# Kernel optimization log

Hardware: AMD Instinct MI355X
Metric: run time of the kernel (lower is better)

Reference implementation:

```python
import jax, jax.numpy as jnp
import numpy as np

NUM_EXPERTS = 8
NUM_LANGS = 4
TOP_K = 2
D_MODEL = 1024
EXPERT_SIZE = 4096
B, S = 2, 2048


def setup_inputs() -> dict:
    key = jax.random.key(0)
    ks = jax.random.split(key, 6)
    def xavier(k, shape, fan_in, fan_out):
        a = float(np.sqrt(6.0 / (fan_in + fan_out)))
        return jax.random.uniform(k, shape, jnp.float32, -a, a)
    return {
        "x": jax.random.normal(ks[0], (B, S, D_MODEL), jnp.float32),
        "router_w": xavier(ks[1], (NUM_EXPERTS, D_MODEL), D_MODEL, NUM_EXPERTS),
        "router_b": jnp.zeros((NUM_EXPERTS,), jnp.float32),
        "lang_w": xavier(ks[2], (NUM_LANGS, D_MODEL), D_MODEL, NUM_LANGS),
        "lang_b": jnp.zeros((NUM_LANGS,), jnp.float32),
        "w1": xavier(ks[3], (NUM_EXPERTS, D_MODEL, EXPERT_SIZE), D_MODEL, EXPERT_SIZE),
        "b1": jnp.zeros((NUM_EXPERTS, EXPERT_SIZE), jnp.float32),
        "w2": xavier(ks[4], (NUM_EXPERTS, EXPERT_SIZE, D_MODEL), EXPERT_SIZE, D_MODEL),
        "b2": jnp.zeros((NUM_EXPERTS, D_MODEL), jnp.float32),
    }


def reference(x, router_w, router_b, lang_w, lang_b, w1, b1, w2, b2):
    # Language-aware routing bias
    lang_logits = x @ lang_w.T + lang_b                      # [B,S,L]
    lang_probs = jax.nn.softmax(lang_logits, axis=-1)
    # lang_probs[..., idx:idx+2].sum(-1): slice may be width 1 at the edge,
    # emulate with a zero pad column.
    lp_pad = jnp.pad(lang_probs, ((0, 0), (0, 0), (0, 1)))
    idx = jnp.arange(NUM_EXPERTS) % NUM_LANGS                # [E]
    expert_weights = lp_pad[..., idx] + lp_pad[..., idx + 1] # [B,S,E]

    router_logits = x @ router_w.T + router_b + 0.1 * expert_weights
    router_probs = jax.nn.softmax(router_logits, axis=-1)   # [B,S,E]
    top_p, top_i = jax.lax.top_k(router_probs, TOP_K)        # [B,S,K]
    top_p = top_p / top_p.sum(axis=-1, keepdims=True)

    # Dense per-expert MLP (dropout=0 / eval). torch GELU default = exact erf.
    h = jax.nn.gelu(jnp.einsum('bsd,edh->bseh', x, w1) + b1, approximate=False)
    expert_out = jnp.einsum('bseh,ehd->bsed', h, w2) + b2    # [B,S,E,D]

    sel = jnp.take_along_axis(expert_out, top_i[..., None], axis=2)  # [B,S,K,D]
    return (top_p[..., None] * sel).sum(axis=2)              # [B,S,D]
```

## Files before the change

kernel.cpp:

```cpp
#include <hip/hip_runtime.h>
#include <cstdint>
#include <cstddef>

#define T_TOK 4096
#define DM 1024
#define HS 4096
#define NE 8
#define MAXROWS 9216
#define MAXTILES 72

typedef __attribute__((ext_vector_type(8))) short short8;
typedef __attribute__((ext_vector_type(4))) float floatx4;

__device__ __forceinline__ unsigned short f2bf(float f) {
  union { float f; unsigned u; } v; v.f = f;
  unsigned r = (v.u + 0x7fffu + ((v.u >> 16) & 1u)) >> 16;
  return (unsigned short)r;
}

__device__ __forceinline__ void gload_lds16(const void* g, void* l) {
  __builtin_amdgcn_global_load_lds((const __attribute__((address_space(1))) void*)g,
                                   (__attribute__((address_space(3))) void*)l, 16, 0, 0);
}


__global__ void k_init(int* counts, int* cursor, unsigned* list) {
  int i = blockIdx.x * 256 + threadIdx.x;
  if (i < NE) { counts[i] = 0; cursor[i] = 0; }
  if (i < MAXROWS) list[i] = 0xFFFFFFFFu;
}

__global__ void k_route(const float* __restrict__ x, const float* __restrict__ rw,
                        const float* __restrict__ rb, const float* __restrict__ lw,
                        const float* __restrict__ lb, int* __restrict__ top_i,
                        float* __restrict__ top_p, int* __restrict__ counts) {
  int t = blockIdx.x * 4 + (threadIdx.x >> 6);
  int lane = threadIdx.x & 63;
  const float4* xt = (const float4*)(x + (size_t)t * DM);
  float4 xv[4];
#pragma unroll
  for (int j = 0; j < 4; j++) xv[j] = xt[lane * 4 + j];
  float dots[12];
#pragma unroll
  for (int r = 0; r < 12; r++) {
    const float4* wr = (const float4*)(r < 4 ? lw + r * DM : rw + (r - 4) * DM);
    float s = 0.f;
#pragma unroll
    for (int j = 0; j < 4; j++) {
      float4 w = wr[lane * 4 + j];
      s += xv[j].x * w.x + xv[j].y * w.y + xv[j].z * w.z + xv[j].w * w.w;
    }
#pragma unroll
    for (int o = 32; o > 0; o >>= 1) s += __shfl_xor(s, o, 64);
    dots[r] = s;
  }
  if (lane == 0) {
    float lp[4]; float m = -1e30f;
#pragma unroll
    for (int i = 0; i < 4; i++) { lp[i] = dots[i] + lb[i]; m = fmaxf(m, lp[i]); }
    float sum = 0.f;
#pragma unroll
    for (int i = 0; i < 4; i++) { lp[i] = expf(lp[i] - m); sum += lp[i]; }
#pragma unroll
    for (int i = 0; i < 4; i++) lp[i] /= sum;
    float ew[4];
    ew[0] = lp[0] + lp[1]; ew[1] = lp[1] + lp[2]; ew[2] = lp[2] + lp[3]; ew[3] = lp[3];
    float r8[8];
#pragma unroll
    for (int e = 0; e < 8; e++) r8[e] = dots[4 + e] + rb[e] + 0.1f * ew[e & 3];
    int e0 = 0;
#pragma unroll
    for (int e = 1; e < 8; e++) if (r8[e] > r8[e0]) e0 = e;
    int e1 = (e0 == 0) ? 1 : 0;
#pragma unroll
    for (int e = 0; e < 8; e++) if (e != e0 && r8[e] > r8[e1]) e1 = e;
    float tt = expf(r8[e1] - r8[e0]);
    float w0 = 1.f / (1.f + tt);
    float w1 = tt / (1.f + tt);
    top_i[t * 2] = e0; top_i[t * 2 + 1] = e1;
    top_p[t * 2] = w0; top_p[t * 2 + 1] = w1;
    atomicAdd(&counts[e0], 1); atomicAdd(&counts[e1], 1);
  }
}

__global__ void k_offsets(const int* counts, int* off) {
  if (threadIdx.x == 0) {
    int acc = 0;
    for (int e = 0; e < NE; e++) {
      off[e] = acc;
      int p = ((counts[e] + 127) >> 7) << 7;
      acc += p;
    }
    off[NE] = acc;
  }
}

__global__ void k_scatter(const int* __restrict__ top_i, const int* __restrict__ off,
                          int* cursor, unsigned* __restrict__ list) {
  int t = blockIdx.x * 256 + threadIdx.x;
  if (t >= T_TOK) return;
#pragma unroll
  for (int k = 0; k < 2; k++) {
    int e = top_i[t * 2 + k];
    int pos = atomicAdd(&cursor[e], 1);
    list[off[e] + pos] = (unsigned)(t * 2 + k);
  }
}

__global__ void k_cvt_x(const float* __restrict__ x, unsigned short* __restrict__ xb) {
  int i = blockIdx.x * 256 + threadIdx.x;
  float4 v = ((const float4*)x)[i];
  union { unsigned short us[4]; uint2 u2; } o;
  o.us[0] = f2bf(v.x); o.us[1] = f2bf(v.y); o.us[2] = f2bf(v.z); o.us[3] = f2bf(v.w);
  ((uint2*)xb)[i] = o.u2;
}

__global__ void k_transpose_bf16(const float* __restrict__ src, unsigned short* __restrict__ dst,
                                 int K, int N) {
  __shared__ float tile[64][65];
  const float* s = src + (size_t)blockIdx.z * K * N;
  unsigned short* d = dst + (size_t)blockIdx.z * K * N;
  int n0 = blockIdx.x * 64, k0 = blockIdx.y * 64;
  int tr = threadIdx.x >> 4;
  int tc = (threadIdx.x & 15) * 4;
#pragma unroll
  for (int j = 0; j < 4; j++) {
    int row = tr + j * 16;
    float4 v = *(const float4*)&s[(size_t)(k0 + row) * N + n0 + tc];
    tile[row][tc + 0] = v.x; tile[row][tc + 1] = v.y;
    tile[row][tc + 2] = v.z; tile[row][tc + 3] = v.w;
  }
  __syncthreads();
#pragma unroll
  for (int j = 0; j < 4; j++) {
    int n = tr + j * 16;
    union { unsigned short us[4]; uint2 u2; } o;
#pragma unroll
    for (int i = 0; i < 4; i++) o.us[i] = f2bf(tile[tc + i][n]);
    *(uint2*)&d[(size_t)(n0 + n) * K + k0 + tc] = o.u2;
  }
}

__global__ void k_init_out(const int* __restrict__ top_i, const float* __restrict__ top_p,
                           const float* __restrict__ b2, float* __restrict__ out) {
  int i = blockIdx.x * 256 + threadIdx.x;
  int t = i >> 10, d = i & 1023;
  int e0 = top_i[t * 2], e1 = top_i[t * 2 + 1];
  out[i] = top_p[t * 2] * b2[e0 * DM + d] + top_p[t * 2 + 1] * b2[e1 * DM + d];
}

template <int MODE>
__global__ __launch_bounds__(256, 4) void k_gemm(
    const unsigned short* __restrict__ Abase,
    const unsigned short* __restrict__ Wt,
    const int* __restrict__ off, const unsigned* __restrict__ list,
    const float* __restrict__ b1, const float* __restrict__ top_p,
    unsigned short* __restrict__ Hout, float* __restrict__ out,
    int K, int N) {
  int nx = gridDim.x;
  int flat = blockIdx.y * nx + blockIdx.x;
  int cpx = (nx * gridDim.y) >> 3;
  int swz = (flat & 7) * cpx + (flat >> 3);
  int n0 = (swz % nx) * 128;
  int r0 = (swz / nx) * 128;

  int total = off[NE];
  if (r0 >= total) return;
  int e = 0;
  while (r0 >= off[e + 1]) ++e;

  __shared__ __align__(16) unsigned short lA[2][128 * 32];
  __shared__ __align__(16) unsigned short lB[2][128 * 32];
  __shared__ float sP[128];
  __shared__ int sTok[128];

  int tid = threadIdx.x;
  int srow = tid >> 2;
  int key_s = (srow >> 1) & 3;
  int koff_src = (((tid & 3) ^ key_s) * 8);
  int kdst = (tid & 3) * 8;

  const unsigned short* srcA[2];
#pragma unroll
  for (int c = 0; c < 2; c++) {
    int row = c * 64 + srow;
    size_t arow;
    if (MODE == 0) {
      unsigned pair = list[r0 + row];
      arow = (pair == 0xFFFFFFFFu) ? 0 : (size_t)(pair >> 1);
    } else {
      arow = (size_t)(r0 + row);
    }
    srcA[c] = Abase + arow * K + koff_src;
  }
  const unsigned short* srcB[2];
#pragma unroll
  for (int c = 0; c < 2; c++)
    srcB[c] = Wt + ((size_t)e * N + n0 + c * 64 + srow) * K + koff_src;

  if (MODE == 1 && tid < 128) {
    unsigned pair = list[r0 + tid];
    if (pair == 0xFFFFFFFFu) { sTok[tid] = -1; sP[tid] = 0.f; }
    else { sTok[tid] = (int)(pair >> 1); sP[tid] = top_p[pair]; }
  }

  floatx4 acc[4][4] = {};
  int lane = tid & 63;
  int w = tid >> 6;
  int wm = w >> 1, wn = w & 1;
  int lr = lane & 15, kq = lane >> 4;
  int kx = kq ^ ((lr >> 1) & 3);

#define STAGE(BUF, KK)                                                        \
  do {                                                                        \
    _Pragma("unroll")                                                         \
    for (int c = 0; c < 2; c++) {                                             \
      gload_lds16(srcA[c] + (KK), &lA[BUF][(c * 64 + srow) * 32 + kdst]);     \
      gload_lds16(srcB[c] + (KK), &lB[BUF][(c * 64 + srow) * 32 + kdst]);     \
    }                                                                         \
  } while (0)

  STAGE(0, 0);
  __syncthreads();

  int cur = 0;
  for (int k0 = 0; k0 < K; k0 += 32) {
    if (k0 + 32 < K) STAGE(cur ^ 1, k0 + 32);
    const short8* pA = (const short8*)lA[cur];
    const short8* pB = (const short8*)lB[cur];
    short8 a[4], b[4];
#pragma unroll
    for (int i = 0; i < 4; i++) a[i] = pA[(wm * 64 + i * 16 + lr) * 4 + kx];
#pragma unroll
    for (int j = 0; j < 4; j++) b[j] = pB[(wn * 64 + j * 16 + lr) * 4 + kx];
#pragma unroll
    for (int i = 0; i < 4; i++)
#pragma unroll
      for (int j = 0; j < 4; j++)
        acc[i][j] = __builtin_amdgcn_mfma_f32_16x16x32_bf16(a[i], b[j], acc[i][j], 0, 0, 0);
    __syncthreads();
    cur ^= 1;
  }
#undef STAGE

  int rbase = wm * 64 + kq * 4;
  int cbase = wn * 64 + lr;
  if (MODE == 0) {
#pragma unroll
    for (int i = 0; i < 4; i++)
#pragma unroll
      for (int j = 0; j < 4; j++)
#pragma unroll
        for (int g = 0; g < 4; g++) {
          int row = rbase + i * 16 + g;
          int col = cbase + j * 16;
          float v = acc[i][j][g] + b1[e * HS + n0 + col];
          v = 0.5f * v * (1.f + erff(v * 0.70710678118f));
          Hout[(size_t)(r0 + row) * (size_t)N + n0 + col] = f2bf(v);
        }
  } else {
#pragma unroll
    for (int i = 0; i < 4; i++)
#pragma unroll
      for (int j = 0; j < 4; j++)
#pragma unroll
        for (int g = 0; g < 4; g++) {
          int row = rbase + i * 16 + g;
          int col = cbase + j * 16;
          int tok = sTok[row];
          if (tok >= 0)
            atomicAdd(&out[(size_t)tok * DM + n0 + col], sP[row] * acc[i][j][g]);
        }
  }
}


extern "C" void kernel_launch(void* const* d_in, const int* in_sizes, int n_in,
                              void* d_out, int out_size, void* d_ws, size_t ws_size,
                              hipStream_t stream) {
  const float* x  = (const float*)d_in[0];
  const float* rw = (const float*)d_in[1];
  const float* rb = (const float*)d_in[2];
  const float* lw = (const float*)d_in[3];
  const float* lb = (const float*)d_in[4];
  const float* w1 = (const float*)d_in[5];
  const float* b1 = (const float*)d_in[6];
  const float* w2 = (const float*)d_in[7];
  const float* b2 = (const float*)d_in[8];
  float* out = (float*)d_out;
  char* ws = (char*)d_ws;

  int* counts = (int*)ws;
  int* cursor = (int*)(ws + 32);
  int* off    = (int*)(ws + 64);
  int* top_i  = (int*)(ws + 128);
  float* top_p = (float*)(ws + 128 + 32768);
  unsigned* list = (unsigned*)(ws + 65792);
  unsigned short* xb = (unsigned short*)(ws + 102912);
  unsigned short* wt = (unsigned short*)(ws + 102912 + 8388608);
  unsigned short* h  = (unsigned short*)(ws + 102912 + 8388608 + 67108864);

  k_init<<<dim3((MAXROWS + 255) / 256), dim3(256), 0, stream>>>(counts, cursor, list);
  k_route<<<dim3(T_TOK / 4), dim3(256), 0, stream>>>(x, rw, rb, lw, lb, top_i, top_p, counts);
  k_offsets<<<dim3(1), dim3(64), 0, stream>>>(counts, off);
  k_scatter<<<dim3(T_TOK / 256), dim3(256), 0, stream>>>(top_i, off, cursor, list);
  k_cvt_x<<<dim3(T_TOK * DM / 4 / 256), dim3(256), 0, stream>>>(x, xb);
  k_transpose_bf16<<<dim3(HS / 64, DM / 64, NE), dim3(256), 0, stream>>>(w1, wt, DM, HS);
  k_gemm<0><<<dim3(HS / 128, MAXTILES), dim3(256), 0, stream>>>(
      xb, wt, off, list, b1, top_p, h, nullptr, DM, HS);
  k_transpose_bf16<<<dim3(DM / 64, HS / 64, NE), dim3(256), 0, stream>>>(w2, wt, HS, DM);
  k_init_out<<<dim3(T_TOK * DM / 256), dim3(256), 0, stream>>>(top_i, top_p, b2, out);
  k_gemm<1><<<dim3(DM / 128, MAXTILES), dim3(256), 0, stream>>>(
      h, wt, off, list, nullptr, top_p, nullptr, out, HS, DM);
}
```

Before: 515.4 us.

## Triple-buffer GEMM pipeline, split-K the second GEMM, fuse x conversion, tanh GELU

The GEMM now uses three LDS stages with explicit vmcnt waits and split A/B staging interleaved with MFMA groups under s_setprio. K and N become template constants. The second GEMM is split four ways along K across gridDim.z to add parallelism, and its results are still combined through atomics. The x-to-bf16 conversion is fused into the init kernel, and the exact erf GELU is replaced with a tanh approximation, which changes numerics and may not match the reference.

Measured after the change: 541.5 us. 1.05x slower.

```diff
diff --git a/kernel.cpp b/kernel.cpp
--- a/kernel.cpp
+++ b/kernel.cpp
@@ -24,10 +24,15 @@
 }
 
 
-__global__ void k_init(int* counts, int* cursor, unsigned* list) {
+__global__ void k_cvt_init(const float* __restrict__ x, unsigned short* __restrict__ xb,
+                           int* counts, int* cursor, unsigned* list) {
   int i = blockIdx.x * 256 + threadIdx.x;
   if (i < NE) { counts[i] = 0; cursor[i] = 0; }
   if (i < MAXROWS) list[i] = 0xFFFFFFFFu;
+  float4 v = ((const float4*)x)[i];
+  union { unsigned short us[4]; uint2 u2; } o;
+  o.us[0] = f2bf(v.x); o.us[1] = f2bf(v.y); o.us[2] = f2bf(v.z); o.us[3] = f2bf(v.w);
+  ((uint2*)xb)[i] = o.u2;
 }
 
 __global__ void k_route(const float* __restrict__ x, const float* __restrict__ rw,
@@ -107,14 +112,6 @@
   }
 }
 
-__global__ void k_cvt_x(const float* __restrict__ x, unsigned short* __restrict__ xb) {
-  int i = blockIdx.x * 256 + threadIdx.x;
-  float4 v = ((const float4*)x)[i];
-  union { unsigned short us[4]; uint2 u2; } o;
-  o.us[0] = f2bf(v.x); o.us[1] = f2bf(v.y); o.us[2] = f2bf(v.z); o.us[3] = f2bf(v.w);
-  ((uint2*)xb)[i] = o.u2;
-}
-
 __global__ void k_transpose_bf16(const float* __restrict__ src, unsigned short* __restrict__ dst,
                                  int K, int N) {
   __shared__ float tile[64][65];
@@ -149,36 +146,39 @@
   out[i] = top_p[t * 2] * b2[e0 * DM + d] + top_p[t * 2 + 1] * b2[e1 * DM + d];
 }
 
-template <int MODE>
-__global__ __launch_bounds__(256, 4) void k_gemm(
+template <int MODE, int K, int N, int KT>
+__global__ __launch_bounds__(256, 3) void k_gemm(
     const unsigned short* __restrict__ Abase,
     const unsigned short* __restrict__ Wt,
     const int* __restrict__ off, const unsigned* __restrict__ list,
-    const float* __restrict__ b1, const float* __restrict__ top_p,
-    unsigned short* __restrict__ Hout, float* __restrict__ out,
-    int K, int N) {
-  int nx = gridDim.x;
-  int flat = blockIdx.y * nx + blockIdx.x;
-  int cpx = (nx * gridDim.y) >> 3;
+    const float* __restrict__ bias, const float* __restrict__ top_p,
+    unsigned short* __restrict__ Hout, float* __restrict__ out) {
+  int gx = gridDim.x, gy = gridDim.y;
+  int flat = (blockIdx.z * gy + blockIdx.y) * gx + blockIdx.x;
+  int nwg = gx * gy * gridDim.z;
+  int cpx = nwg >> 3;
   int swz = (flat & 7) * cpx + (flat >> 3);
-  int n0 = (swz % nx) * 128;
-  int r0 = (swz / nx) * 128;
+  int bn = swz % gx; int rest = swz / gx;
+  int bm = rest % gy; int zz = rest / gy;
+  int n0 = bn * 128;
+  int r0 = bm * 128;
+  int kb = zz * (KT * 32);
 
   int total = off[NE];
   if (r0 >= total) return;
   int e = 0;
   while (r0 >= off[e + 1]) ++e;
 
-  __shared__ __align__(16) unsigned short lA[2][128 * 32];
-  __shared__ __align__(16) unsigned short lB[2][128 * 32];
+  __shared__ __align__(16) unsigned short lA[3][128 * 32];
+  __shared__ __align__(16) unsigned short lB[3][128 * 32];
   __shared__ float sP[128];
   __shared__ int sTok[128];
 
   int tid = threadIdx.x;
   int srow = tid >> 2;
-  int key_s = (srow >> 1) & 3;
-  int koff_src = (((tid & 3) ^ key_s) * 8);
-  int kdst = (tid & 3) * 8;
+  int skey = (srow >> 1) & 3;
+  int koff_src = ((tid & 3) ^ skey) * 8;
+  int ldst = srow * 32 + (tid & 3) * 8;
 
   const unsigned short* srcA[2];
 #pragma unroll
@@ -191,12 +191,12 @@
     } else {
       arow = (size_t)(r0 + row);
     }
-    srcA[c] = Abase + arow * K + koff_src;
+    srcA[c] = Abase + arow * K + kb + koff_src;
   }
   const unsigned short* srcB[2];
 #pragma unroll
   for (int c = 0; c < 2; c++)
-    srcB[c] = Wt + ((size_t)e * N + n0 + c * 64 + srow) * K + koff_src;
+    srcB[c] = Wt + ((size_t)e * N + n0 + c * 64 + srow) * K + kb + koff_src;
 
   if (MODE == 1 && tid < 128) {
     unsigned pair = list[r0 + tid];
@@ -210,38 +210,66 @@
   int wm = w >> 1, wn = w & 1;
   int lr = lane & 15, kq = lane >> 4;
   int kx = kq ^ ((lr >> 1) & 3);
-
-#define STAGE(BUF, KK)                                                        \
+  int aBase = (wm * 64 + lr) * 4 + kx;
+  int bBase = (wn * 64 + lr) * 4 + kx;
+
+#define STAGE_A(BUF, TT)                                                      \
   do {                                                                        \
     _Pragma("unroll")                                                         \
-    for (int c = 0; c < 2; c++) {                                             \
-      gload_lds16(srcA[c] + (KK), &lA[BUF][(c * 64 + srow) * 32 + kdst]);     \
-      gload_lds16(srcB[c] + (KK), &lB[BUF][(c * 64 + srow) * 32 + kdst]);     \
-    }                                                                         \
+    for (int c = 0; c < 2; c++)                                               \
+      gload_lds16(srcA[c] + (size_t)(TT) * 32, &lA[BUF][c * 2048 + ldst]);    \
   } while (0)
-
-  STAGE(0, 0);
+#define STAGE_B(BUF, TT)                                                      \
+  do {                                                                        \
+    _Pragma("unroll")                                                         \
+    for (int c = 0; c < 2; c++)                                               \
+      gload_lds16(srcB[c] + (size_t)(TT) * 32, &lB[BUF][c * 2048 + ldst]);    \
+  } while (0)
+
   __syncthreads();
 
-  int cur = 0;
-  for (int k0 = 0; k0 < K; k0 += 32) {
-    if (k0 + 32 < K) STAGE(cur ^ 1, k0 + 32);
+  STAGE_A(0, 0); STAGE_B(0, 0);
+  STAGE_A(1, 1); STAGE_B(1, 1);
+  asm volatile("s_waitcnt vmcnt(4)\ns_barrier" ::: "memory");
+
+  int cur = 0, nxt = 2;
+  for (int t = 0; t < KT; ++t) {
     const short8* pA = (const short8*)lA[cur];
     const short8* pB = (const short8*)lB[cur];
-    short8 a[4], b[4];
-#pragma unroll
-    for (int i = 0; i < 4; i++) a[i] = pA[(wm * 64 + i * 16 + lr) * 4 + kx];
-#pragma unroll
-    for (int j = 0; j < 4; j++) b[j] = pB[(wn * 64 + j * 16 + lr) * 4 + kx];
-#pragma unroll
-    for (int i = 0; i < 4; i++)
-#pragma unroll
-      for (int j = 0; j < 4; j++)
-        acc[i][j] = __builtin_amdgcn_mfma_f32_16x16x32_bf16(a[i], b[j], acc[i][j], 0, 0, 0);
-    __syncthreads();
-    cur ^= 1;
-  }
-#undef STAGE
+    bool pf = (t + 2 < KT);
+    if (pf) STAGE_A(nxt, t + 2);
+    short8 a0[4], b0[2];
+#pragma unroll
+    for (int m = 0; m < 4; m++) a0[m] = pA[aBase + m * 64];
+#pragma unroll
+    for (int n = 0; n < 2; n++) b0[n] = pB[bBase + n * 64];
+    __builtin_amdgcn_s_setprio(1);
+#pragma unroll
+    for (int m = 0; m < 4; m++)
+#pragma unroll
+      for (int n = 0; n < 2; n++)
+        acc[m][n] = __builtin_amdgcn_mfma_f32_16x16x32_bf16(a0[m], b0[n], acc[m][n], 0, 0, 0);
+    __builtin_amdgcn_s_setprio(0);
+    if (pf) STAGE_B(nxt, t + 2);
+    short8 b1v[2];
+#pragma unroll
+    for (int n = 0; n < 2; n++) b1v[n] = pB[bBase + (n + 2) * 64];
+    __builtin_amdgcn_s_setprio(1);
+#pragma unroll
+    for (int m = 0; m < 4; m++)
+#pragma unroll
+      for (int n = 0; n < 2; n++)
+        acc[m][n + 2] = __builtin_amdgcn_mfma_f32_16x16x32_bf16(a0[m], b1v[n], acc[m][n + 2], 0, 0, 0);
+    __builtin_amdgcn_s_setprio(0);
+    if (t + 1 < KT) {
+      if (pf) asm volatile("s_waitcnt vmcnt(4)\ns_barrier" ::: "memory");
+      else    asm volatile("s_waitcnt vmcnt(0)\ns_barrier" ::: "memory");
+    }
+    cur = (cur == 2) ? 0 : cur + 1;
+    nxt = (nxt == 2) ? 0 : nxt + 1;
+  }
+#undef STAGE_A
+#undef STAGE_B
 
   int rbase = wm * 64 + kq * 4;
   int cbase = wn * 64 + lr;
@@ -254,9 +282,10 @@
         for (int g = 0; g < 4; g++) {
           int row = rbase + i * 16 + g;
           int col = cbase + j * 16;
-          float v = acc[i][j][g] + b1[e * HS + n0 + col];
-          v = 0.5f * v * (1.f + erff(v * 0.70710678118f));
-          Hout[(size_t)(r0 + row) * (size_t)N + n0 + col] = f2bf(v);
+          float v = acc[i][j][g] + bias[e * N + n0 + col];
+          float u = v * (0.7978845608f + 0.0356774081f * v * v);
+          float gl = v / (1.f + __expf(-2.f * u));
+          Hout[(size_t)(r0 + row) * (size_t)N + n0 + col] = f2bf(gl);
         }
   } else {
 #pragma unroll
@@ -300,16 +329,15 @@
   unsigned short* wt = (unsigned short*)(ws + 102912 + 8388608);
   unsigned short* h  = (unsigned short*)(ws + 102912 + 8388608 + 67108864);
 
-  k_init<<<dim3((MAXROWS + 255) / 256), dim3(256), 0, stream>>>(counts, cursor, list);
+  k_cvt_init<<<dim3(T_TOK * DM / 4 / 256), dim3(256), 0, stream>>>(x, xb, counts, cursor, list);
   k_route<<<dim3(T_TOK / 4), dim3(256), 0, stream>>>(x, rw, rb, lw, lb, top_i, top_p, counts);
   k_offsets<<<dim3(1), dim3(64), 0, stream>>>(counts, off);
   k_scatter<<<dim3(T_TOK / 256), dim3(256), 0, stream>>>(top_i, off, cursor, list);
-  k_cvt_x<<<dim3(T_TOK * DM / 4 / 256), dim3(256), 0, stream>>>(x, xb);
   k_transpose_bf16<<<dim3(HS / 64, DM / 64, NE), dim3(256), 0, stream>>>(w1, wt, DM, HS);
-  k_gemm<0><<<dim3(HS / 128, MAXTILES), dim3(256), 0, stream>>>(
-      xb, wt, off, list, b1, top_p, h, nullptr, DM, HS);
+  k_init_out<<<dim3(T_TOK * DM / 256), dim3(256), 0, stream>>>(top_i, top_p, b2, out);
+  k_gemm<0, DM, HS, DM / 32><<<dim3(HS / 128, MAXTILES, 1), dim3(256), 0, stream>>>(
+      xb, wt, off, list, b1, top_p, h, nullptr);
   k_transpose_bf16<<<dim3(DM / 64, HS / 64, NE), dim3(256), 0, stream>>>(w2, wt, HS, DM);
-  k_init_out<<<dim3(T_TOK * DM / 256), dim3(256), 0, stream>>>(top_i, top_p, b2, out);
-  k_gemm<1><<<dim3(DM / 128, MAXTILES), dim3(256), 0, stream>>>(
-      h, wt, off, list, nullptr, top_p, nullptr, out, HS, DM);
-}
+  k_gemm<1, HS, DM, HS / 4 / 32><<<dim3(DM / 128, MAXTILES, 4), dim3(256), 0, stream>>>(
+      h, wt, off, list, nullptr, top_p, nullptr, out);
+}
```

## Fuse routing kernels, load gathered A from global, use tanh GELU

Applied to the files above, without the earlier changes.

Merges x bf16 conversion into the routing kernel, and merges offset computation and scatter into one single-block kernel. Replaces the init kernel with memsets. Splits the templated GEMM into two kernels. The first GEMM now reads gathered A rows directly from global memory into registers instead of staging them through LDS. It also replaces the exact erf GELU with a tanh/sigmoid approximation, which changes numerics relative to the reference's exact GELU. Together these aim to cut launch overhead, LDS traffic and epilogue cost.

New measurement: 583.9 us. 13.3% more time.

```diff
diff --git a/kernel.cpp b/kernel.cpp
--- a/kernel.cpp
+++ b/kernel.cpp
@@ -23,17 +23,19 @@
                                    (__attribute__((address_space(3))) void*)l, 16, 0, 0);
 }
 
-
-__global__ void k_init(int* counts, int* cursor, unsigned* list) {
-  int i = blockIdx.x * 256 + threadIdx.x;
-  if (i < NE) { counts[i] = 0; cursor[i] = 0; }
-  if (i < MAXROWS) list[i] = 0xFFFFFFFFu;
-}
-
-__global__ void k_route(const float* __restrict__ x, const float* __restrict__ rw,
-                        const float* __restrict__ rb, const float* __restrict__ lw,
-                        const float* __restrict__ lb, int* __restrict__ top_i,
-                        float* __restrict__ top_p, int* __restrict__ counts) {
+__global__ void k_cvt_route(const float* __restrict__ x, unsigned short* __restrict__ xb,
+                            const float* __restrict__ rw, const float* __restrict__ rb,
+                            const float* __restrict__ lw, const float* __restrict__ lb,
+                            int* __restrict__ top_i, float* __restrict__ top_p,
+                            int* __restrict__ counts) {
+#pragma unroll
+  for (int j = 0; j < 4; j++) {
+    int i = blockIdx.x * 1024 + j * 256 + threadIdx.x;
+    float4 v = ((const float4*)x)[i];
+    union { unsigned short us[4]; uint2 u2; } o;
+    o.us[0] = f2bf(v.x); o.us[1] = f2bf(v.y); o.us[2] = f2bf(v.z); o.us[3] = f2bf(v.w);
+    ((uint2*)xb)[i] = o.u2;
+  }
   int t = blockIdx.x * 4 + (threadIdx.x >> 6);
   int lane = threadIdx.x & 63;
   const float4* xt = (const float4*)(x + (size_t)t * DM);
@@ -83,36 +85,26 @@
   }
 }
 
-__global__ void k_offsets(const int* counts, int* off) {
+__global__ void k_offscatter(const int* __restrict__ counts, int* __restrict__ off,
+                             const int* __restrict__ top_i, int* cursor,
+                             unsigned* __restrict__ list) {
   if (threadIdx.x == 0) {
     int acc = 0;
     for (int e = 0; e < NE; e++) {
       off[e] = acc;
-      int p = ((counts[e] + 127) >> 7) << 7;
-      acc += p;
+      acc += ((counts[e] + 127) >> 7) << 7;
     }
     off[NE] = acc;
   }
-}
-
-__global__ void k_scatter(const int* __restrict__ top_i, const int* __restrict__ off,
-                          int* cursor, unsigned* __restrict__ list) {
-  int t = blockIdx.x * 256 + threadIdx.x;
-  if (t >= T_TOK) return;
-#pragma unroll
-  for (int k = 0; k < 2; k++) {
-    int e = top_i[t * 2 + k];
-    int pos = atomicAdd(&cursor[e], 1);
-    list[off[e] + pos] = (unsigned)(t * 2 + k);
-  }
-}
-
-__global__ void k_cvt_x(const float* __restrict__ x, unsigned short* __restrict__ xb) {
-  int i = blockIdx.x * 256 + threadIdx.x;
-  float4 v = ((const float4*)x)[i];
-  union { unsigned short us[4]; uint2 u2; } o;
-  o.us[0] = f2bf(v.x); o.us[1] = f2bf(v.y); o.us[2] = f2bf(v.z); o.us[3] = f2bf(v.w);
-  ((uint2*)xb)[i] = o.u2;
+  __syncthreads();
+  for (int t = threadIdx.x; t < T_TOK; t += 1024) {
+#pragma unroll
+    for (int k = 0; k < 2; k++) {
+      int e = top_i[t * 2 + k];
+      int pos = atomicAdd(&cursor[e], 1);
+      list[off[e] + pos] = (unsigned)(t * 2 + k);
+    }
+  }
 }
 
 __global__ void k_transpose_bf16(const float* __restrict__ src, unsigned short* __restrict__ dst,
@@ -149,14 +141,12 @@
   out[i] = top_p[t * 2] * b2[e0 * DM + d] + top_p[t * 2 + 1] * b2[e1 * DM + d];
 }
 
-template <int MODE>
-__global__ __launch_bounds__(256, 4) void k_gemm(
+__global__ __launch_bounds__(256, 4) void k_gemm1(
     const unsigned short* __restrict__ Abase,
     const unsigned short* __restrict__ Wt,
     const int* __restrict__ off, const unsigned* __restrict__ list,
-    const float* __restrict__ b1, const float* __restrict__ top_p,
-    unsigned short* __restrict__ Hout, float* __restrict__ out,
-    int K, int N) {
+    const float* __restrict__ bias, unsigned short* __restrict__ Hout) {
+  const int K = DM, N = HS;
   int nx = gridDim.x;
   int flat = blockIdx.y * nx + blockIdx.x;
   int cpx = (nx * gridDim.y) >> 3;
@@ -169,6 +159,101 @@
   int e = 0;
   while (r0 >= off[e + 1]) ++e;
 
+  __shared__ __align__(16) unsigned short lB[2][128 * 32];
+
+  int tid = threadIdx.x;
+  int srow = tid >> 2;
+  int key_s = (srow >> 1) & 3;
+  int koff_src = ((tid & 3) ^ key_s) * 8;
+  int kdst = (tid & 3) * 8;
+
+  const unsigned short* srcB[2];
+#pragma unroll
+  for (int c = 0; c < 2; c++)
+    srcB[c] = Wt + ((size_t)e * N + n0 + c * 64 + srow) * K + koff_src;
+
+  int lane = tid & 63;
+  int w = tid >> 6;
+  int wm = w >> 1, wn = w & 1;
+  int lr = lane & 15, kq = lane >> 4;
+  int kx = kq ^ ((lr >> 1) & 3);
+
+  unsigned aoff[4];
+#pragma unroll
+  for (int i = 0; i < 4; i++) {
+    int row = r0 + wm * 64 + i * 16 + lr;
+    unsigned pair = list[row];
+    unsigned arow = (pair == 0xFFFFFFFFu) ? 0u : (pair >> 1);
+    aoff[i] = arow * (unsigned)K + (unsigned)(kq * 8);
+  }
+
+  floatx4 acc[4][4] = {};
+
+#define STAGEB(BUF, KK)                                                       \
+  do {                                                                        \
+    _Pragma("unroll")                                                         \
+    for (int c = 0; c < 2; c++)                                               \
+      gload_lds16(srcB[c] + (KK), &lB[BUF][(c * 64 + srow) * 32 + kdst]);     \
+  } while (0)
+
+  STAGEB(0, 0);
+  __syncthreads();
+
+  int cur = 0;
+  for (int k0 = 0; k0 < K; k0 += 32) {
+    if (k0 + 32 < K) STAGEB(cur ^ 1, k0 + 32);
+    const short8* pB = (const short8*)lB[cur];
+    short8 a[4], b[4];
+#pragma unroll
+    for (int i = 0; i < 4; i++)
+      a[i] = *(const short8*)(Abase + aoff[i] + k0);
+#pragma unroll
+    for (int j = 0; j < 4; j++) b[j] = pB[(wn * 64 + j * 16 + lr) * 4 + kx];
+#pragma unroll
+    for (int i = 0; i < 4; i++)
+#pragma unroll
+      for (int j = 0; j < 4; j++)
+        acc[i][j] = __builtin_amdgcn_mfma_f32_16x16x32_bf16(a[i], b[j], acc[i][j], 0, 0, 0);
+    __syncthreads();
+    cur ^= 1;
+  }
+#undef STAGEB
+
+  int rbase = wm * 64 + kq * 4;
+  int cbase = wn * 64 + lr;
+#pragma unroll
+  for (int i = 0; i < 4; i++)
+#pragma unroll
+    for (int j = 0; j < 4; j++)
+#pragma unroll
+      for (int g = 0; g < 4; g++) {
+        int row = rbase + i * 16 + g;
+        int col = cbase + j * 16;
+        float v = acc[i][j][g] + bias[e * N + n0 + col];
+        float u = v * (0.7978845608f + 0.0356774081f * v * v);
+        float gl = v / (1.f + __expf(-2.f * u));
+        Hout[(size_t)(r0 + row) * (size_t)N + n0 + col] = f2bf(gl);
+      }
+}
+
+__global__ __launch_bounds__(256, 4) void k_gemm2(
+    const unsigned short* __restrict__ Abase,
+    const unsigned short* __restrict__ Wt,
+    const int* __restrict__ off, const unsigned* __restrict__ list,
+    const float* __restrict__ top_p, float* __restrict__ out) {
+  const int K = HS, N = DM;
+  int nx = gridDim.x;
+  int flat = blockIdx.y * nx + blockIdx.x;
+  int cpx = (nx * gridDim.y) >> 3;
+  int swz = (flat & 7) * cpx + (flat >> 3);
+  int n0 = (swz % nx) * 128;
+  int r0 = (swz / nx) * 128;
+
+  int total = off[NE];
+  if (r0 >= total) return;
+  int e = 0;
+  while (r0 >= off[e + 1]) ++e;
+
   __shared__ __align__(16) unsigned short lA[2][128 * 32];
   __shared__ __align__(16) unsigned short lB[2][128 * 32];
   __shared__ float sP[128];
@@ -177,28 +262,19 @@
   int tid = threadIdx.x;
   int srow = tid >> 2;
   int key_s = (srow >> 1) & 3;
-  int koff_src = (((tid & 3) ^ key_s) * 8);
+  int koff_src = ((tid & 3) ^ key_s) * 8;
   int kdst = (tid & 3) * 8;
 
   const unsigned short* srcA[2];
 #pragma unroll
-  for (int c = 0; c < 2; c++) {
-    int row = c * 64 + srow;
-    size_t arow;
-    if (MODE == 0) {
-      unsigned pair = list[r0 + row];
-      arow = (pair == 0xFFFFFFFFu) ? 0 : (size_t)(pair >> 1);
-    } else {
-      arow = (size_t)(r0 + row);
-    }
-    srcA[c] = Abase + arow * K + koff_src;
-  }
+  for (int c = 0; c < 2; c++)
+    srcA[c] = Abase + (size_t)(r0 + c * 64 + srow) * K + koff_src;
   const unsigned short* srcB[2];
 #pragma unroll
   for (int c = 0; c < 2; c++)
     srcB[c] = Wt + ((size_t)e * N + n0 + c * 64 + srow) * K + koff_src;
 
-  if (MODE == 1 && tid < 128) {
+  if (tid < 128) {
     unsigned pair = list[r0 + tid];
     if (pair == 0xFFFFFFFFu) { sTok[tid] = -1; sP[tid] = 0.f; }
     else { sTok[tid] = (int)(pair >> 1); sP[tid] = top_p[pair]; }
@@ -245,33 +321,18 @@
 
   int rbase = wm * 64 + kq * 4;
   int cbase = wn * 64 + lr;
-  if (MODE == 0) {
-#pragma unroll
-    for (int i = 0; i < 4; i++)
-#pragma unroll
-      for (int j = 0; j < 4; j++)
-#pragma unroll
-        for (int g = 0; g < 4; g++) {
-          int row = rbase + i * 16 + g;
-          int col = cbase + j * 16;
-          float v = acc[i][j][g] + b1[e * HS + n0 + col];
-          v = 0.5f * v * (1.f + erff(v * 0.70710678118f));
-          Hout[(size_t)(r0 + row) * (size_t)N + n0 + col] = f2bf(v);
-        }
-  } else {
-#pragma unroll
-    for (int i = 0; i < 4; i++)
-#pragma unroll
-      for (int j = 0; j < 4; j++)
-#pragma unroll
-        for (int g = 0; g < 4; g++) {
-          int row = rbase + i * 16 + g;
-          int col = cbase + j * 16;
-          int tok = sTok[row];
-          if (tok >= 0)
-            atomicAdd(&out[(size_t)tok * DM + n0 + col], sP[row] * acc[i][j][g]);
-        }
-  }
+#pragma unroll
+  for (int i = 0; i < 4; i++)
+#pragma unroll
+    for (int j = 0; j < 4; j++)
+#pragma unroll
+      for (int g = 0; g < 4; g++) {
+        int row = rbase + i * 16 + g;
+        int col = cbase + j * 16;
+        int tok = sTok[row];
+        if (tok >= 0)
+          atomicAdd(&out[(size_t)tok * DM + n0 + col], sP[row] * acc[i][j][g]);
+      }
 }
 
 
@@ -300,16 +361,16 @@
   unsigned short* wt = (unsigned short*)(ws + 102912 + 8388608);
   unsigned short* h  = (unsigned short*)(ws + 102912 + 8388608 + 67108864);
 
-  k_init<<<dim3((MAXROWS + 255) / 256), dim3(256), 0, stream>>>(counts, cursor, list);
-  k_route<<<dim3(T_TOK / 4), dim3(256), 0, stream>>>(x, rw, rb, lw, lb, top_i, top_p, counts);
-  k_offsets<<<dim3(1), dim3(64), 0, stream>>>(counts, off);
-  k_scatter<<<dim3(T_TOK / 256), dim3(256), 0, stream>>>(top_i, off, cursor, list);
-  k_cvt_x<<<dim3(T_TOK * DM / 4 / 256), dim3(256), 0, stream>>>(x, xb);
+  hipMemsetAsync(ws, 0, 128, stream);
+  hipMemsetAsync(list, 0xFF, MAXROWS * 4, stream);
+  k_cvt_route<<<dim3(T_TOK / 4), dim3(256), 0, stream>>>(
+      x, xb, rw, rb, lw, lb, top_i, top_p, counts);
+  k_offscatter<<<dim3(1), dim3(1024), 0, stream>>>(counts, off, top_i, cursor, list);
   k_transpose_bf16<<<dim3(HS / 64, DM / 64, NE), dim3(256), 0, stream>>>(w1, wt, DM, HS);
-  k_gemm<0><<<dim3(HS / 128, MAXTILES), dim3(256), 0, stream>>>(
-      xb, wt, off, list, b1, top_p, h, nullptr, DM, HS);
+  k_init_out<<<dim3(T_TOK * DM / 256), dim3(256), 0, stream>>>(top_i, top_p, b2, out);
+  k_gemm1<<<dim3(HS / 128, MAXTILES), dim3(256), 0, stream>>>(
+      xb, wt, off, list, b1, h);
   k_transpose_bf16<<<dim3(DM / 64, HS / 64, NE), dim3(256), 0, stream>>>(w2, wt, HS, DM);
-  k_init_out<<<dim3(T_TOK * DM / 256), dim3(256), 0, stream>>>(top_i, top_p, b2, out);
-  k_gemm<1><<<dim3(DM / 128, MAXTILES), dim3(256), 0, stream>>>(
-      h, wt, off, list, nullptr, top_p, nullptr, out, HS, DM);
-}
+  k_gemm2<<<dim3(DM / 128, MAXTILES), dim3(256), 0, stream>>>(
+      h, wt, off, list, top_p, out);
+}
```

## Fuse small setup kernels, widen weight transpose, vectorize init, use tanh GELU

Applied to the files above, without the earlier changes.

Merges the bf16 conversion of x into the routing kernel and folds the offset and scatter steps into one 1024-thread kernel. The init kernel is replaced with memsets. The fp32-to-bf16 weight transpose now works on 128x128 tiles, packs bf16 pairs with an XOR-swizzled LDS layout and writes 16-byte stores. The output-init kernel is vectorized to float4. The exact erf GELU in the first GEMM epilogue is replaced by a tanh-style approximation through __expf, which trades accuracy for fewer instructions.

New measurement: 523.8 us. No clear change (+1.6%).

```diff
diff --git a/kernel.cpp b/kernel.cpp
--- a/kernel.cpp
+++ b/kernel.cpp
@@ -23,17 +23,19 @@
                                    (__attribute__((address_space(3))) void*)l, 16, 0, 0);
 }
 
-
-__global__ void k_init(int* counts, int* cursor, unsigned* list) {
-  int i = blockIdx.x * 256 + threadIdx.x;
-  if (i < NE) { counts[i] = 0; cursor[i] = 0; }
-  if (i < MAXROWS) list[i] = 0xFFFFFFFFu;
-}
-
-__global__ void k_route(const float* __restrict__ x, const float* __restrict__ rw,
-                        const float* __restrict__ rb, const float* __restrict__ lw,
-                        const float* __restrict__ lb, int* __restrict__ top_i,
-                        float* __restrict__ top_p, int* __restrict__ counts) {
+__global__ void k_cvt_route(const float* __restrict__ x, unsigned short* __restrict__ xb,
+                            const float* __restrict__ rw, const float* __restrict__ rb,
+                            const float* __restrict__ lw, const float* __restrict__ lb,
+                            int* __restrict__ top_i, float* __restrict__ top_p,
+                            int* __restrict__ counts) {
+#pragma unroll
+  for (int j = 0; j < 4; j++) {
+    int i = blockIdx.x * 1024 + j * 256 + threadIdx.x;
+    float4 v = ((const float4*)x)[i];
+    union { unsigned short us[4]; uint2 u2; } o;
+    o.us[0] = f2bf(v.x); o.us[1] = f2bf(v.y); o.us[2] = f2bf(v.z); o.us[3] = f2bf(v.w);
+    ((uint2*)xb)[i] = o.u2;
+  }
   int t = blockIdx.x * 4 + (threadIdx.x >> 6);
   int lane = threadIdx.x & 63;
   const float4* xt = (const float4*)(x + (size_t)t * DM);
@@ -83,70 +85,74 @@
   }
 }
 
-__global__ void k_offsets(const int* counts, int* off) {
+__global__ void k_offscatter(const int* __restrict__ counts, int* __restrict__ off,
+                             const int* __restrict__ top_i, int* cursor,
+                             unsigned* __restrict__ list) {
   if (threadIdx.x == 0) {
     int acc = 0;
     for (int e = 0; e < NE; e++) {
       off[e] = acc;
-      int p = ((counts[e] + 127) >> 7) << 7;
-      acc += p;
+      acc += ((counts[e] + 127) >> 7) << 7;
     }
     off[NE] = acc;
   }
-}
-
-__global__ void k_scatter(const int* __restrict__ top_i, const int* __restrict__ off,
-                          int* cursor, unsigned* __restrict__ list) {
-  int t = blockIdx.x * 256 + threadIdx.x;
-  if (t >= T_TOK) return;
-#pragma unroll
-  for (int k = 0; k < 2; k++) {
-    int e = top_i[t * 2 + k];
-    int pos = atomicAdd(&cursor[e], 1);
-    list[off[e] + pos] = (unsigned)(t * 2 + k);
-  }
-}
-
-__global__ void k_cvt_x(const float* __restrict__ x, unsigned short* __restrict__ xb) {
-  int i = blockIdx.x * 256 + threadIdx.x;
-  float4 v = ((const float4*)x)[i];
-  union { unsigned short us[4]; uint2 u2; } o;
-  o.us[0] = f2bf(v.x); o.us[1] = f2bf(v.y); o.us[2] = f2bf(v.z); o.us[3] = f2bf(v.w);
-  ((uint2*)xb)[i] = o.u2;
-}
-
-__global__ void k_transpose_bf16(const float* __restrict__ src, unsigned short* __restrict__ dst,
-                                 int K, int N) {
-  __shared__ float tile[64][65];
+  __syncthreads();
+  for (int t = threadIdx.x; t < T_TOK; t += 1024) {
+#pragma unroll
+    for (int k = 0; k < 2; k++) {
+      int e = top_i[t * 2 + k];
+      int pos = atomicAdd(&cursor[e], 1);
+      list[off[e] + pos] = (unsigned)(t * 2 + k);
+    }
+  }
+}
+
+template <int K, int N>
+__global__ __launch_bounds__(256) void k_transpose2(const float* __restrict__ src,
+                                                    unsigned short* __restrict__ dst) {
+  __shared__ unsigned tile[128][68];
   const float* s = src + (size_t)blockIdx.z * K * N;
   unsigned short* d = dst + (size_t)blockIdx.z * K * N;
-  int n0 = blockIdx.x * 64, k0 = blockIdx.y * 64;
-  int tr = threadIdx.x >> 4;
-  int tc = (threadIdx.x & 15) * 4;
-#pragma unroll
-  for (int j = 0; j < 4; j++) {
-    int row = tr + j * 16;
-    float4 v = *(const float4*)&s[(size_t)(k0 + row) * N + n0 + tc];
-    tile[row][tc + 0] = v.x; tile[row][tc + 1] = v.y;
-    tile[row][tc + 2] = v.z; tile[row][tc + 3] = v.w;
+  int n0 = blockIdx.x * 128, k0 = blockIdx.y * 128;
+  int tid = threadIdx.x;
+  int nc4 = (tid & 31) * 4;
+  int kg = tid >> 5;
+#pragma unroll
+  for (int j = 0; j < 8; j++) {
+    int kp = kg + 8 * j;
+    int k = 2 * kp;
+    float4 a = *(const float4*)&s[(size_t)(k0 + k) * N + n0 + nc4];
+    float4 b = *(const float4*)&s[(size_t)(k0 + k + 1) * N + n0 + nc4];
+    const float* fa = (const float*)&a;
+    const float* fb = (const float*)&b;
+#pragma unroll
+    for (int i = 0; i < 4; i++) {
+      int n = nc4 + i;
+      int v = ((n >> 3) & 15) << 2;
+      tile[n][kp ^ v] = (unsigned)f2bf(fa[i]) | ((unsigned)f2bf(fb[i]) << 16);
+    }
   }
   __syncthreads();
-#pragma unroll
-  for (int j = 0; j < 4; j++) {
-    int n = tr + j * 16;
-    union { unsigned short us[4]; uint2 u2; } o;
-#pragma unroll
-    for (int i = 0; i < 4; i++) o.us[i] = f2bf(tile[tc + i][n]);
-    *(uint2*)&d[(size_t)(n0 + n) * K + k0 + tc] = o.u2;
+  int h = tid & 15;
+#pragma unroll
+  for (int j = 0; j < 8; j++) {
+    int n = (tid >> 4) + 16 * j;
+    int v = ((n >> 3) & 15) << 2;
+    uint4 q = *(const uint4*)&tile[n][(4 * h) ^ v];
+    *(uint4*)&d[(size_t)(n0 + n) * K + k0 + 8 * h] = q;
   }
 }
 
 __global__ void k_init_out(const int* __restrict__ top_i, const float* __restrict__ top_p,
-                           const float* __restrict__ b2, float* __restrict__ out) {
+                           const float* __restrict__ b2, float4* __restrict__ out) {
   int i = blockIdx.x * 256 + threadIdx.x;
-  int t = i >> 10, d = i & 1023;
+  int t = i >> 8, d4 = i & 255;
   int e0 = top_i[t * 2], e1 = top_i[t * 2 + 1];
-  out[i] = top_p[t * 2] * b2[e0 * DM + d] + top_p[t * 2 + 1] * b2[e1 * DM + d];
+  float p0 = top_p[t * 2], p1 = top_p[t * 2 + 1];
+  float4 b0 = ((const float4*)(b2 + e0 * DM))[d4];
+  float4 b1 = ((const float4*)(b2 + e1 * DM))[d4];
+  out[i] = make_float4(p0 * b0.x + p1 * b1.x, p0 * b0.y + p1 * b1.y,
+                       p0 * b0.z + p1 * b1.z, p0 * b0.w + p1 * b1.w);
 }
 
 template <int MODE>
@@ -154,7 +160,7 @@
     const unsigned short* __restrict__ Abase,
     const unsigned short* __restrict__ Wt,
     const int* __restrict__ off, const unsigned* __restrict__ list,
-    const float* __restrict__ b1, const float* __restrict__ top_p,
+    const float* __restrict__ bias, const float* __restrict__ top_p,
     unsigned short* __restrict__ Hout, float* __restrict__ out,
     int K, int N) {
   int nx = gridDim.x;
@@ -177,7 +183,7 @@
   int tid = threadIdx.x;
   int srow = tid >> 2;
   int key_s = (srow >> 1) & 3;
-  int koff_src = (((tid & 3) ^ key_s) * 8);
+  int koff_src = ((tid & 3) ^ key_s) * 8;
   int kdst = (tid & 3) * 8;
 
   const unsigned short* srcA[2];
@@ -254,9 +260,10 @@
         for (int g = 0; g < 4; g++) {
           int row = rbase + i * 16 + g;
           int col = cbase + j * 16;
-          float v = acc[i][j][g] + b1[e * HS + n0 + col];
-          v = 0.5f * v * (1.f + erff(v * 0.70710678118f));
-          Hout[(size_t)(r0 + row) * (size_t)N + n0 + col] = f2bf(v);
+          float v = acc[i][j][g] + bias[e * N + n0 + col];
+          float u = v * (0.7978845608f + 0.0356774081f * v * v);
+          float gl = v / (1.f + __expf(-2.f * u));
+          Hout[(size_t)(r0 + row) * (size_t)N + n0 + col] = f2bf(gl);
         }
   } else {
 #pragma unroll
@@ -295,21 +302,22 @@
   int* off    = (int*)(ws + 64);
   int* top_i  = (int*)(ws + 128);
   float* top_p = (float*)(ws + 128 + 32768);
-  unsigned* list = (unsigned*)(ws + 65792);
-  unsigned short* xb = (unsigned short*)(ws + 102912);
-  unsigned short* wt = (unsigned short*)(ws + 102912 + 8388608);
-  unsigned short* h  = (unsigned short*)(ws + 102912 + 8388608 + 67108864);
-
-  k_init<<<dim3((MAXROWS + 255) / 256), dim3(256), 0, stream>>>(counts, cursor, list);
-  k_route<<<dim3(T_TOK / 4), dim3(256), 0, stream>>>(x, rw, rb, lw, lb, top_i, top_p, counts);
-  k_offsets<<<dim3(1), dim3(64), 0, stream>>>(counts, off);
-  k_scatter<<<dim3(T_TOK / 256), dim3(256), 0, stream>>>(top_i, off, cursor, list);
-  k_cvt_x<<<dim3(T_TOK * DM / 4 / 256), dim3(256), 0, stream>>>(x, xb);
-  k_transpose_bf16<<<dim3(HS / 64, DM / 64, NE), dim3(256), 0, stream>>>(w1, wt, DM, HS);
+  unsigned* list = (unsigned*)(ws + 128 + 65536);
+  unsigned short* xb = (unsigned short*)(ws + 131072);
+  unsigned short* wt = (unsigned short*)(ws + 131072 + 8388608);
+  unsigned short* h  = (unsigned short*)(ws + 131072 + 8388608 + 67108864);
+
+  hipMemsetAsync(ws, 0, 128, stream);
+  hipMemsetAsync(list, 0xFF, MAXROWS * 4, stream);
+  k_cvt_route<<<dim3(T_TOK / 4), dim3(256), 0, stream>>>(
+      x, xb, rw, rb, lw, lb, top_i, top_p, counts);
+  k_offscatter<<<dim3(1), dim3(1024), 0, stream>>>(counts, off, top_i, cursor, list);
+  k_transpose2<DM, HS><<<dim3(HS / 128, DM / 128, NE), dim3(256), 0, stream>>>(w1, wt);
+  k_init_out<<<dim3(T_TOK * DM / 4 / 256), dim3(256), 0, stream>>>(
+      top_i, top_p, b2, (float4*)out);
   k_gemm<0><<<dim3(HS / 128, MAXTILES), dim3(256), 0, stream>>>(
       xb, wt, off, list, b1, top_p, h, nullptr, DM, HS);
-  k_transpose_bf16<<<dim3(DM / 64, HS / 64, NE), dim3(256), 0, stream>>>(w2, wt, HS, DM);
-  k_init_out<<<dim3(T_TOK * DM / 256), dim3(256), 0, stream>>>(top_i, top_p, b2, out);
+  k_transpose2<HS, DM><<<dim3(DM / 128, HS / 128, NE), dim3(256), 0, stream>>>(w2, wt);
   k_gemm<1><<<dim3(DM / 128, MAXTILES), dim3(256), 0, stream>>>(
       h, wt, off, list, nullptr, top_p, nullptr, out, HS, DM);
 }
```
